# Kernel optimization log

Measured on AMD Instinct MI355X. Metric: run time of the kernel, lower is better.

## Reference

```python
import jax, jax.numpy as jnp
import numpy as np

MIN_BOX_SIZE = 0.05


def setup_inputs() -> dict:
    key = jax.random.key(0)
    mask_fg = jax.random.uniform(key, (256, 1, 512, 512), dtype=jnp.float32)
    return {"mask_fg": mask_fg}


def reference(mask_fg):
    # mask_fg: (B, 1, H, W). Returns boxes: (B, 4) as [x0, y0, x1, y1] in [0, 1].
    B, _, H, W = mask_fg.shape
    m = mask_fg[:, 0] > 0.5  # (B, H, W) boolean foreground mask

    row_any = jnp.any(m, axis=2)  # (B, H): row contains a foreground pixel
    col_any = jnp.any(m, axis=1)  # (B, W): col contains a foreground pixel
    empty = ~jnp.any(row_any, axis=1)  # (B,): no foreground at all

    ys = jnp.arange(H, dtype=jnp.float32)
    xs = jnp.arange(W, dtype=jnp.float32)

    # masked min/max of row / column indices, normalized (matches torch: idx / H, idx / W)
    y_min = jnp.min(jnp.where(row_any, ys, jnp.float32(H)), axis=1) / H
    y_max = jnp.max(jnp.where(row_any, ys, jnp.float32(-1)), axis=1) / H
    x_min = jnp.min(jnp.where(col_any, xs, jnp.float32(W)), axis=1) / W
    x_max = jnp.max(jnp.where(col_any, xs, jnp.float32(-1)), axis=1) / W

    s = jnp.float32(MIN_BOX_SIZE)

    def expand(lo, hi):
        too_small = (hi - lo) < s
        c = (lo + hi) * 0.5
        lo2 = jnp.maximum(jnp.float32(0.0), c - s * 0.5)
        hi2 = jnp.minimum(jnp.float32(1.0), c + s * 0.5)
        return jnp.where(too_small, lo2, lo), jnp.where(too_small, hi2, hi)

    x_min, x_max = expand(x_min, x_max)
    y_min, y_max = expand(y_min, y_max)

    boxes = jnp.stack([x_min, y_min, x_max, y_max], axis=1)  # (B, 4)
    default = jnp.array([0.25, 0.25, 0.75, 0.75], dtype=jnp.float32)
    boxes = jnp.where(empty[:, None], default[None, :], boxes)
    return boxes
```

## Files before the change

kernel.cpp:

```cpp
#include <hip/hip_runtime.h>


constexpr int H = 512;
constexpr int W = 512;
constexpr int THREADS = 1024;

__global__ __launch_bounds__(THREADS)
void bbox_kernel(const float* __restrict__ mask, float* __restrict__ out) {
    const int b = blockIdx.x;
    const float4* __restrict__ base =
        reinterpret_cast<const float4*>(mask) + (size_t)b * (H * W / 4);
    const int t = threadIdx.x;

    int ymin = H, ymax = -1, xmin = W, xmax = -1;

    #pragma unroll
    for (int i = 0; i < 64; i += 8) {
        float4 v[8];
        #pragma unroll
        for (int j = 0; j < 8; ++j) v[j] = base[t + (i + j) * THREADS];
        #pragma unroll
        for (int j = 0; j < 8; ++j) {
            const int e = (t + (i + j) * THREADS) * 4;
            const int y = e >> 9;
            const int x = e & (W - 1);
            const bool a0 = v[j].x > 0.5f;
            const bool a1 = v[j].y > 0.5f;
            const bool a2 = v[j].z > 0.5f;
            const bool a3 = v[j].w > 0.5f;
            if (a0 | a1 | a2 | a3) { ymin = min(ymin, y); ymax = max(ymax, y); }
            if (a0) { xmin = min(xmin, x    ); xmax = max(xmax, x    ); }
            if (a1) { xmin = min(xmin, x + 1); xmax = max(xmax, x + 1); }
            if (a2) { xmin = min(xmin, x + 2); xmax = max(xmax, x + 2); }
            if (a3) { xmin = min(xmin, x + 3); xmax = max(xmax, x + 3); }
        }
    }

    #pragma unroll
    for (int off = 32; off > 0; off >>= 1) {
        ymin = min(ymin, __shfl_down(ymin, off));
        ymax = max(ymax, __shfl_down(ymax, off));
        xmin = min(xmin, __shfl_down(xmin, off));
        xmax = max(xmax, __shfl_down(xmax, off));
    }

    __shared__ int s_ymin[16], s_ymax[16], s_xmin[16], s_xmax[16];
    const int wave = t >> 6;
    if ((t & 63) == 0) {
        s_ymin[wave] = ymin; s_ymax[wave] = ymax;
        s_xmin[wave] = xmin; s_xmax[wave] = xmax;
    }
    __syncthreads();

    if (t == 0) {
        #pragma unroll
        for (int w = 1; w < 16; ++w) {
            ymin = min(ymin, s_ymin[w]); ymax = max(ymax, s_ymax[w]);
            xmin = min(xmin, s_xmin[w]); xmax = max(xmax, s_xmax[w]);
        }
        float x0, y0, x1, y1;
        if (ymax < 0) {
            x0 = 0.25f; y0 = 0.25f; x1 = 0.75f; y1 = 0.75f;
        } else {
            y0 = (float)ymin * (1.0f / H);
            y1 = (float)ymax * (1.0f / H);
            x0 = (float)xmin * (1.0f / W);
            x1 = (float)xmax * (1.0f / W);
            const float s = 0.05f;
            if (x1 - x0 < s) {
                const float c = (x0 + x1) * 0.5f;
                x0 = fmaxf(0.0f, c - s * 0.5f);
                x1 = fminf(1.0f, c + s * 0.5f);
            }
            if (y1 - y0 < s) {
                const float c = (y0 + y1) * 0.5f;
                y0 = fmaxf(0.0f, c - s * 0.5f);
                y1 = fminf(1.0f, c + s * 0.5f);
            }
        }
        reinterpret_cast<float4*>(out)[b] = make_float4(x0, y0, x1, y1);
    }
}

extern "C" void kernel_launch(void* const* d_in, const int* in_sizes, int n_in,
                              void* d_out, int out_size, void* d_ws, size_t ws_size,
                              hipStream_t stream) {
    const float* mask = (const float*)d_in[0];
    float* out = (float*)d_out;
    const int B = in_sizes[0] / (H * W);
    bbox_kernel<<<B, THREADS, 0, stream>>>(mask, out);
}
```

Measured before the change: 351.8 us.

## Replace full-image scan with early-exit edge searches for bounding box

```diff
diff --git a/kernel.cpp b/kernel.cpp
--- a/kernel.cpp
+++ b/kernel.cpp
@@ -4,79 +4,119 @@
 constexpr int H = 512;
 constexpr int W = 512;
 constexpr int THREADS = 1024;
+constexpr int NWAVE = THREADS / 64;
+constexpr int BIG = 1 << 29;
+
+__device__ __forceinline__ int block_min(int v, int t, int* s_tmp, int* s_res) {
+    #pragma unroll
+    for (int off = 32; off > 0; off >>= 1) v = min(v, __shfl_down(v, off));
+    if ((t & 63) == 0) s_tmp[t >> 6] = v;
+    __syncthreads();
+    if (t == 0) {
+        int m = s_tmp[0];
+        #pragma unroll
+        for (int w = 1; w < NWAVE; ++w) m = min(m, s_tmp[w]);
+        *s_res = m;
+    }
+    __syncthreads();
+    return *s_res;
+}
+
+__device__ __forceinline__ int block_max(int v, int t, int* s_tmp, int* s_res) {
+    #pragma unroll
+    for (int off = 32; off > 0; off >>= 1) v = max(v, __shfl_down(v, off));
+    if ((t & 63) == 0) s_tmp[t >> 6] = v;
+    __syncthreads();
+    if (t == 0) {
+        int m = s_tmp[0];
+        #pragma unroll
+        for (int w = 1; w < NWAVE; ++w) m = max(m, s_tmp[w]);
+        *s_res = m;
+    }
+    __syncthreads();
+    return *s_res;
+}
 
 __global__ __launch_bounds__(THREADS)
 void bbox_kernel(const float* __restrict__ mask, float* __restrict__ out) {
     const int b = blockIdx.x;
-    const float4* __restrict__ base =
+    const float4* __restrict__ img =
         reinterpret_cast<const float4*>(mask) + (size_t)b * (H * W / 4);
     const int t = threadIdx.x;
+    __shared__ int s_tmp[NWAVE];
+    __shared__ int s_res;
 
-    int ymin = H, ymax = -1, xmin = W, xmax = -1;
+    const int rg = t >> 7;
+    const int cg = t & 127;
+    const int rs = t >> 1;
+    const int cs = t & 1;
 
-    #pragma unroll
-    for (int i = 0; i < 64; i += 8) {
-        float4 v[8];
-        #pragma unroll
-        for (int j = 0; j < 8; ++j) v[j] = base[t + (i + j) * THREADS];
-        #pragma unroll
-        for (int j = 0; j < 8; ++j) {
-            const int e = (t + (i + j) * THREADS) * 4;
-            const int y = e >> 9;
-            const int x = e & (W - 1);
-            const bool a0 = v[j].x > 0.5f;
-            const bool a1 = v[j].y > 0.5f;
-            const bool a2 = v[j].z > 0.5f;
-            const bool a3 = v[j].w > 0.5f;
-            if (a0 | a1 | a2 | a3) { ymin = min(ymin, y); ymax = max(ymax, y); }
-            if (a0) { xmin = min(xmin, x    ); xmax = max(xmax, x    ); }
-            if (a1) { xmin = min(xmin, x + 1); xmax = max(xmax, x + 1); }
-            if (a2) { xmin = min(xmin, x + 2); xmax = max(xmax, x + 2); }
-            if (a3) { xmin = min(xmin, x + 3); xmax = max(xmax, x + 3); }
-        }
+    int ymin = BIG;
+    for (int g = 0; g < H / 8; ++g) {
+        const int r = g * 8 + rg;
+        const float4 v = img[(r << 7) + cg];
+        const bool fg = (v.x > 0.5f) || (v.y > 0.5f) || (v.z > 0.5f) || (v.w > 0.5f);
+        const int res = block_min(fg ? r : BIG, t, s_tmp, &s_res);
+        if (res < BIG) { ymin = res; break; }
+    }
+    if (ymin >= BIG) {
+        if (t == 0)
+            reinterpret_cast<float4*>(out)[b] = make_float4(0.25f, 0.25f, 0.75f, 0.75f);
+        return;
     }
 
-    #pragma unroll
-    for (int off = 32; off > 0; off >>= 1) {
-        ymin = min(ymin, __shfl_down(ymin, off));
-        ymax = max(ymax, __shfl_down(ymax, off));
-        xmin = min(xmin, __shfl_down(xmin, off));
-        xmax = max(xmax, __shfl_down(xmax, off));
+    int ymax = -1;
+    for (int g = H / 8 - 1; g >= (ymin >> 3); --g) {
+        const int r = g * 8 + rg;
+        const float4 v = img[(r << 7) + cg];
+        const bool fg = (v.x > 0.5f) || (v.y > 0.5f) || (v.z > 0.5f) || (v.w > 0.5f);
+        const int res = block_max(fg ? r : -1, t, s_tmp, &s_res);
+        if (res >= 0) { ymax = res; break; }
     }
 
-    __shared__ int s_ymin[16], s_ymax[16], s_xmin[16], s_xmax[16];
-    const int wave = t >> 6;
-    if ((t & 63) == 0) {
-        s_ymin[wave] = ymin; s_ymax[wave] = ymax;
-        s_xmin[wave] = xmin; s_xmax[wave] = xmax;
+    int xmin = BIG;
+    for (int s = 0; s < W / 8; ++s) {
+        const int c4 = s * 2 + cs;
+        const float4 v = img[(rs << 7) + c4];
+        const int c = c4 * 4;
+        int cand = BIG;
+        if (v.w > 0.5f) cand = c + 3;
+        if (v.z > 0.5f) cand = c + 2;
+        if (v.y > 0.5f) cand = c + 1;
+        if (v.x > 0.5f) cand = c;
+        const int res = block_min(cand, t, s_tmp, &s_res);
+        if (res < BIG) { xmin = res; break; }
     }
-    __syncthreads();
+
+    int xmax = -1;
+    for (int s = W / 8 - 1; s >= (xmin >> 3); --s) {
+        const int c4 = s * 2 + cs;
+        const float4 v = img[(rs << 7) + c4];
+        const int c = c4 * 4;
+        int cand = -1;
+        if (v.x > 0.5f) cand = c;
+        if (v.y > 0.5f) cand = c + 1;
+        if (v.z > 0.5f) cand = c + 2;
+        if (v.w > 0.5f) cand = c + 3;
+        const int res = block_max(cand, t, s_tmp, &s_res);
+        if (res >= 0) { xmax = res; break; }
+    }
 
     if (t == 0) {
-        #pragma unroll
-        for (int w = 1; w < 16; ++w) {
-            ymin = min(ymin, s_ymin[w]); ymax = max(ymax, s_ymax[w]);
-            xmin = min(xmin, s_xmin[w]); xmax = max(xmax, s_xmax[w]);
+        float y0 = (float)ymin * (1.0f / H);
+        float y1 = (float)ymax * (1.0f / H);
+        float x0 = (float)xmin * (1.0f / W);
+        float x1 = (float)xmax * (1.0f / W);
+        const float s = 0.05f;
+        if (x1 - x0 < s) {
+            const float c = (x0 + x1) * 0.5f;
+            x0 = fmaxf(0.0f, c - s * 0.5f);
+            x1 = fminf(1.0f, c + s * 0.5f);
         }
-        float x0, y0, x1, y1;
-        if (ymax < 0) {
-            x0 = 0.25f; y0 = 0.25f; x1 = 0.75f; y1 = 0.75f;
-        } else {
-            y0 = (float)ymin * (1.0f / H);
-            y1 = (float)ymax * (1.0f / H);
-            x0 = (float)xmin * (1.0f / W);
-            x1 = (float)xmax * (1.0f / W);
-            const float s = 0.05f;
-            if (x1 - x0 < s) {
-                const float c = (x0 + x1) * 0.5f;
-                x0 = fmaxf(0.0f, c - s * 0.5f);
-                x1 = fminf(1.0f, c + s * 0.5f);
-            }
-            if (y1 - y0 < s) {
-                const float c = (y0 + y1) * 0.5f;
-                y0 = fmaxf(0.0f, c - s * 0.5f);
-                y1 = fminf(1.0f, c + s * 0.5f);
-            }
+        if (y1 - y0 < s) {
+            const float c = (y0 + y1) * 0.5f;
+            y0 = fmaxf(0.0f, c - s * 0.5f);
+            y1 = fminf(1.0f, c + s * 0.5f);
         }
         reinterpret_cast<float4*>(out)[b] = make_float4(x0, y0, x1, y1);
     }
```

Measured after the change: 302.9 us. -13.9%, faster.

## Replace full-image reduction with early-exit directional edge scans per box side

Applied to the files above, without the earlier changes.

```diff
diff --git a/kernel.cpp b/kernel.cpp
--- a/kernel.cpp
+++ b/kernel.cpp
@@ -3,83 +3,106 @@
 
 constexpr int H = 512;
 constexpr int W = 512;
-constexpr int THREADS = 1024;
+constexpr int THREADS = 512;
+constexpr int NWAVE = THREADS / 64;
+constexpr int BIG = 1 << 29;
+
+__device__ __forceinline__ int block_min(int v, int t, int* s_tmp, int* s_res) {
+    #pragma unroll
+    for (int off = 32; off > 0; off >>= 1) v = min(v, __shfl_down(v, off));
+    if ((t & 63) == 0) s_tmp[t >> 6] = v;
+    __syncthreads();
+    if (t == 0) {
+        int m = s_tmp[0];
+        #pragma unroll
+        for (int w = 1; w < NWAVE; ++w) m = min(m, s_tmp[w]);
+        *s_res = m;
+    }
+    __syncthreads();
+    return *s_res;
+}
 
 __global__ __launch_bounds__(THREADS)
-void bbox_kernel(const float* __restrict__ mask, float* __restrict__ out) {
+void scan_kernel(const float* __restrict__ mask, int* __restrict__ ws) {
     const int b = blockIdx.x;
-    const float4* __restrict__ base =
+    const int phase = blockIdx.y;
+    const float4* __restrict__ img =
         reinterpret_cast<const float4*>(mask) + (size_t)b * (H * W / 4);
     const int t = threadIdx.x;
+    __shared__ int s_tmp[NWAVE];
+    __shared__ int s_res;
 
-    int ymin = H, ymax = -1, xmin = W, xmax = -1;
+    int result = BIG;
 
-    #pragma unroll
-    for (int i = 0; i < 64; i += 8) {
-        float4 v[8];
-        #pragma unroll
-        for (int j = 0; j < 8; ++j) v[j] = base[t + (i + j) * THREADS];
-        #pragma unroll
-        for (int j = 0; j < 8; ++j) {
-            const int e = (t + (i + j) * THREADS) * 4;
-            const int y = e >> 9;
-            const int x = e & (W - 1);
-            const bool a0 = v[j].x > 0.5f;
-            const bool a1 = v[j].y > 0.5f;
-            const bool a2 = v[j].z > 0.5f;
-            const bool a3 = v[j].w > 0.5f;
-            if (a0 | a1 | a2 | a3) { ymin = min(ymin, y); ymax = max(ymax, y); }
-            if (a0) { xmin = min(xmin, x    ); xmax = max(xmax, x    ); }
-            if (a1) { xmin = min(xmin, x + 1); xmax = max(xmax, x + 1); }
-            if (a2) { xmin = min(xmin, x + 2); xmax = max(xmax, x + 2); }
-            if (a3) { xmin = min(xmin, x + 3); xmax = max(xmax, x + 3); }
+    if (phase < 2) {
+        const int rr = t >> 7;
+        const int c4 = t & 127;
+        for (int g = 0; g < H / 4; ++g) {
+            const int gg = (phase == 0) ? g : (H / 4 - 1 - g);
+            const int r = gg * 4 + rr;
+            const float4 v = img[(r << 7) + c4];
+            const bool fg = (v.x > 0.5f) || (v.y > 0.5f) ||
+                            (v.z > 0.5f) || (v.w > 0.5f);
+            const int key = fg ? (phase == 0 ? r : -r) : BIG;
+            const int res = block_min(key, t, s_tmp, &s_res);
+            if (res < BIG) { result = res; break; }
+        }
+    } else {
+        const int r = t;
+        for (int s = 0; s < W / 4; ++s) {
+            const int ss = (phase == 2) ? s : (W / 4 - 1 - s);
+            const float4 v = img[(r << 7) + ss];
+            const int c = ss * 4;
+            int key = BIG;
+            if (phase == 2) {
+                if (v.w > 0.5f) key = c + 3;
+                if (v.z > 0.5f) key = c + 2;
+                if (v.y > 0.5f) key = c + 1;
+                if (v.x > 0.5f) key = c;
+            } else {
+                if (v.x > 0.5f) key = -c;
+                if (v.y > 0.5f) key = -(c + 1);
+                if (v.z > 0.5f) key = -(c + 2);
+                if (v.w > 0.5f) key = -(c + 3);
+            }
+            const int res = block_min(key, t, s_tmp, &s_res);
+            if (res < BIG) { result = res; break; }
         }
     }
 
-    #pragma unroll
-    for (int off = 32; off > 0; off >>= 1) {
-        ymin = min(ymin, __shfl_down(ymin, off));
-        ymax = max(ymax, __shfl_down(ymax, off));
-        xmin = min(xmin, __shfl_down(xmin, off));
-        xmax = max(xmax, __shfl_down(xmax, off));
+    if (t == 0) ws[b * 4 + phase] = result;
+}
+
+__global__ __launch_bounds__(256)
+void box_kernel(const int* __restrict__ ws, float* __restrict__ out, int B) {
+    const int b = blockIdx.x * blockDim.x + threadIdx.x;
+    if (b >= B) return;
+    const int ymin = ws[b * 4 + 0];
+    const int nymax = ws[b * 4 + 1];
+    const int xmin = ws[b * 4 + 2];
+    const int nxmax = ws[b * 4 + 3];
+    float x0, y0, x1, y1;
+    if (ymin >= BIG) {
+        x0 = 0.25f; y0 = 0.25f; x1 = 0.75f; y1 = 0.75f;
+    } else {
+        const int ymax = -nymax, xmax = -nxmax;
+        y0 = (float)ymin * (1.0f / H);
+        y1 = (float)ymax * (1.0f / H);
+        x0 = (float)xmin * (1.0f / W);
+        x1 = (float)xmax * (1.0f / W);
+        const float s = 0.05f;
+        if (x1 - x0 < s) {
+            const float c = (x0 + x1) * 0.5f;
+            x0 = fmaxf(0.0f, c - s * 0.5f);
+            x1 = fminf(1.0f, c + s * 0.5f);
+        }
+        if (y1 - y0 < s) {
+            const float c = (y0 + y1) * 0.5f;
+            y0 = fmaxf(0.0f, c - s * 0.5f);
+            y1 = fminf(1.0f, c + s * 0.5f);
+        }
     }
-
-    __shared__ int s_ymin[16], s_ymax[16], s_xmin[16], s_xmax[16];
-    const int wave = t >> 6;
-    if ((t & 63) == 0) {
-        s_ymin[wave] = ymin; s_ymax[wave] = ymax;
-        s_xmin[wave] = xmin; s_xmax[wave] = xmax;
-    }
-    __syncthreads();
-
-    if (t == 0) {
-        #pragma unroll
-        for (int w = 1; w < 16; ++w) {
-            ymin = min(ymin, s_ymin[w]); ymax = max(ymax, s_ymax[w]);
-            xmin = min(xmin, s_xmin[w]); xmax = max(xmax, s_xmax[w]);
-        }
-        float x0, y0, x1, y1;
-        if (ymax < 0) {
-            x0 = 0.25f; y0 = 0.25f; x1 = 0.75f; y1 = 0.75f;
-        } else {
-            y0 = (float)ymin * (1.0f / H);
-            y1 = (float)ymax * (1.0f / H);
-            x0 = (float)xmin * (1.0f / W);
-            x1 = (float)xmax * (1.0f / W);
-            const float s = 0.05f;
-            if (x1 - x0 < s) {
-                const float c = (x0 + x1) * 0.5f;
-                x0 = fmaxf(0.0f, c - s * 0.5f);
-                x1 = fminf(1.0f, c + s * 0.5f);
-            }
-            if (y1 - y0 < s) {
-                const float c = (y0 + y1) * 0.5f;
-                y0 = fmaxf(0.0f, c - s * 0.5f);
-                y1 = fminf(1.0f, c + s * 0.5f);
-            }
-        }
-        reinterpret_cast<float4*>(out)[b] = make_float4(x0, y0, x1, y1);
-    }
+    reinterpret_cast<float4*>(out)[b] = make_float4(x0, y0, x1, y1);
 }
 
 extern "C" void kernel_launch(void* const* d_in, const int* in_sizes, int n_in,
@@ -87,6 +110,9 @@
                               hipStream_t stream) {
     const float* mask = (const float*)d_in[0];
     float* out = (float*)d_out;
+    int* ws = (int*)d_ws;
     const int B = in_sizes[0] / (H * W);
-    bbox_kernel<<<B, THREADS, 0, stream>>>(mask, out);
+    dim3 grid(B, 4);
+    scan_kernel<<<grid, THREADS, 0, stream>>>(mask, ws);
+    box_kernel<<<(B + 255) / 256, 256, 0, stream>>>(ws, out, B);
 }
```

Result: faster. 300.0 us (-14.7%).
